# Optimization experiments

Hardware: AMD Instinct MI355X
Metric: run time of the kernel (lower is better)

The kernel has to match this reference:

```python
import jax, jax.numpy as jnp
import numpy as np

N_TOKEN = 267735
D_PROJ = 1024
CUTOFF_ENDS = [0, 20000, 40000, 200000, 267735]
D_EMBS = [1024, 256, 64, 16]  # d_embed // div_val**i, div_val=4
EMB_SCALE = float(D_PROJ) ** 0.5


def setup_inputs() -> dict:
    key = jax.random.key(0)
    ks = jax.random.split(key, 9)
    inp = jax.random.randint(ks[0], (8, 2048), 0, N_TOKEN)
    d = {"inp": inp}
    for i in range(4):
        size = CUTOFF_ENDS[i + 1] - CUTOFF_ENDS[i]
        de = D_EMBS[i]
        d[f"emb{i}"] = jax.random.normal(ks[1 + 2 * i], (size, de), jnp.float32) * 0.02
        d[f"proj{i}"] = jax.random.normal(ks[2 + 2 * i], (D_PROJ, de), jnp.float32) * 0.02
    return d


def reference(inp, emb0, emb1, emb2, emb3, proj0, proj1, proj2, proj3):
    embs = [emb0, emb1, emb2, emb3]
    projs = [proj0, proj1, proj2, proj3]
    flat = inp.reshape(-1)  # [T]
    out = jnp.zeros((flat.shape[0], D_PROJ), jnp.float32)
    for i in range(4):
        l, r = CUTOFF_ENDS[i], CUTOFF_ENDS[i + 1]
        mask = (flat >= l) & (flat < r)  # clusters are disjoint
        idx = jnp.clip(flat - l, 0, r - l - 1)  # in-range dummy where masked out
        # gather [T, d_emb_i] then project to [T, d_proj] (F.linear with weight [d_proj, d_emb_i])
        e = jnp.einsum('td,pd->tp', embs[i][idx], projs[i])
        out = jnp.where(mask[:, None], e, out)
    return (out * EMB_SCALE).reshape(*inp.shape, D_PROJ)
```

## Files before the change

### kernel.cpp

```cpp
#include <hip/hip_runtime.h>


#define CUT0 20000
#define CUT1 40000
#define CUT2 200000

#define PB1 (1024 * 1024)
#define PB2 (PB1 + 1024 * 256)
#define PB3 (PB2 + 1024 * 64)
#define PBEND (PB3 + 1024 * 32)

typedef __attribute__((ext_vector_type(8))) short bf16x8;
typedef __attribute__((ext_vector_type(8))) unsigned short u16x8;
typedef __attribute__((ext_vector_type(4))) float f32x4;

__device__ __forceinline__ unsigned short f2bf(float f) {
    unsigned u = __float_as_uint(f);
    u += 0x7FFFu + ((u >> 16) & 1u);
    return (unsigned short)(u >> 16);
}

__device__ __forceinline__ u16x8 cvt8(const float* __restrict__ s) {
    float4 a = *(const float4*)s;
    float4 b = *(const float4*)(s + 4);
    return (u16x8){f2bf(a.x), f2bf(a.y), f2bf(a.z), f2bf(a.w),
                   f2bf(b.x), f2bf(b.y), f2bf(b.z), f2bf(b.w)};
}

__device__ __forceinline__ void gl_lds16(const unsigned short* g, unsigned short* s) {
    __builtin_amdgcn_global_load_lds(
        (const __attribute__((address_space(1))) void*)g,
        (__attribute__((address_space(3))) void*)s, 16, 0, 0);
}

__global__ __launch_bounds__(256)
void classify_convert(const int* __restrict__ inp, unsigned* __restrict__ counters,
                      unsigned* __restrict__ lists, int T,
                      const float* __restrict__ proj0, const float* __restrict__ proj1,
                      const float* __restrict__ proj2, const float* __restrict__ proj3,
                      unsigned short* __restrict__ projbf) {
    int t = blockIdx.x * 256 + threadIdx.x;
    int lane = threadIdx.x & 63;
    bool valid = (t < T);
    int id = valid ? inp[t] : 0;
    int c = -1, l = 0;
    if (valid) {
        if (id < CUT0)      { c = 0; l = 0; }
        else if (id < CUT1) { c = 1; l = CUT0; }
        else if (id < CUT2) { c = 2; l = CUT1; }
        else                { c = 3; l = CUT2; }
    }
    #pragma unroll
    for (int i = 0; i < 4; ++i) {
        unsigned long long m = __ballot(c == i);
        if (c == i) {
            int leader = __ffsll(m) - 1;
            unsigned base = 0;
            if (lane == leader) base = atomicAdd(&counters[i], (unsigned)__popcll(m));
            base = __shfl(base, leader);
            unsigned rank = (unsigned)__popcll(m & ((1ull << lane) - 1ull));
            lists[(size_t)i * T + base + rank] = ((unsigned)t << 18) | (unsigned)(id - l);
        }
    }
    const int stride = gridDim.x * 256;
    for (int u = t; u < PBEND / 8; u += stride) {
        int base = u * 8;
        u16x8 o;
        if (base < PB1)       o = cvt8(proj0 + base);
        else if (base < PB2)  o = cvt8(proj1 + (base - PB1));
        else if (base < PB3)  o = cvt8(proj2 + (base - PB2));
        else {
            int rel = base - PB3;
            int row = rel >> 5, col = rel & 31;
            if (col < 16) o = cvt8(proj3 + row * 16 + col);
            else          o = (u16x8){0, 0, 0, 0, 0, 0, 0, 0};
        }
        *(u16x8*)(projbf + base) = o;
    }
}

__global__ __launch_bounds__(256)
void gather_bf16(const float* __restrict__ emb0, const float* __restrict__ emb1,
                 const float* __restrict__ emb2, const float* __restrict__ emb3,
                 const unsigned* __restrict__ lists, const unsigned* __restrict__ counters,
                 int T, unsigned short* __restrict__ ecomp) {
    const int c0 = (int)counters[0], c1 = (int)counters[1];
    const int c2 = (int)counters[2], c3 = (int)counters[3];
    const size_t off1 = (size_t)((c0 + 63) & ~63) * 1024;
    const size_t off2 = off1 + (size_t)((c1 + 63) & ~63) * 256;
    const size_t off3 = off2 + (size_t)((c2 + 63) & ~63) * 64;
    const int n0 = c0 << 7, n1 = c1 << 5, n2 = c2 << 3, n3 = c3 << 2;
    const int total = n0 + n1 + n2 + n3;
    const int stride = gridDim.x * 256;
    for (int u = blockIdx.x * 256 + threadIdx.x; u < total; u += stride) {
        int v = u;
        if (v < n0) {
            int r = v >> 7, j = v & 127;
            unsigned id = lists[r] & 0x3FFFFu;
            *(u16x8*)(ecomp + (size_t)r * 1024 + j * 8) = cvt8(emb0 + (size_t)id * 1024 + j * 8);
        } else if ((v -= n0) < n1) {
            int r = v >> 5, j = v & 31;
            unsigned id = lists[T + r] & 0x3FFFFu;
            *(u16x8*)(ecomp + off1 + (size_t)r * 256 + j * 8) = cvt8(emb1 + (size_t)id * 256 + j * 8);
        } else if ((v -= n1) < n2) {
            int r = v >> 3, j = v & 7;
            unsigned id = lists[2 * T + r] & 0x3FFFFu;
            *(u16x8*)(ecomp + off2 + (size_t)r * 64 + j * 8) = cvt8(emb2 + (size_t)id * 64 + j * 8);
        } else {
            v -= n2;
            int r = v >> 2, j = v & 3;
            unsigned id = lists[3 * T + r] & 0x3FFFFu;
            unsigned short* d = ecomp + off3 + (size_t)r * 32 + j * 8;
            if (j < 2) *(u16x8*)d = cvt8(emb3 + (size_t)id * 16 + j * 8);
            else       *(u16x8*)d = (u16x8){0, 0, 0, 0, 0, 0, 0, 0};
        }
    }
}


template<int KP>
__device__ __forceinline__
void tile_gemm_reg(const unsigned short* __restrict__ E, const unsigned short* __restrict__ P,
                   const unsigned* __restrict__ list, int count, int mtile, int ntile,
                   float* __restrict__ out) {
    constexpr int KST = KP / 32;
    const int m0 = mtile * 64;
    const int rows = min(64, count - m0);
    const int py = ntile * 128;
    const int tid = (int)threadIdx.x;
    const int lane = tid & 63;
    const int w  = tid >> 6;
    const int ln = lane & 15;
    const int qd = lane >> 4;

    const unsigned short* ea = E + (size_t)(m0 + w * 16 + ln) * KP + qd * 8;
    const unsigned short* pb = P + (size_t)(py + ln) * KP + qd * 8;

    f32x4 acc[8];
    #pragma unroll
    for (int ct = 0; ct < 8; ++ct) acc[ct] = (f32x4){0.f, 0.f, 0.f, 0.f};

    #pragma unroll
    for (int s = 0; s < KST; ++s) {
        bf16x8 a = *(const bf16x8*)(ea + s * 32);
        #pragma unroll
        for (int ct = 0; ct < 8; ++ct) {
            bf16x8 b = *(const bf16x8*)(pb + (size_t)ct * 16 * KP + s * 32);
            acc[ct] = __builtin_amdgcn_mfma_f32_16x16x32_bf16(a, b, acc[ct], 0, 0, 0);
        }
    }

    int trow[4];
    #pragma unroll
    for (int r = 0; r < 4; ++r) {
        int row = w * 16 + qd * 4 + r;
        trow[r] = (row < rows) ? (int)(list[m0 + row] >> 18) : -1;
    }
    #pragma unroll
    for (int ct = 0; ct < 8; ++ct)
        #pragma unroll
        for (int r = 0; r < 4; ++r)
            if (trow[r] >= 0)
                out[(size_t)trow[r] * 1024 + py + ct * 16 + ln] = acc[ct][r] * 32.0f;
}

template<int KP>
__device__ __forceinline__
void tile_gemm_lds(const unsigned short* __restrict__ E, const unsigned short* __restrict__ P,
                   const unsigned* __restrict__ list, int count, int mtile, int ntile,
                   float* __restrict__ out,
                   unsigned short* E_s, unsigned short* P_s, unsigned* pk_s) {
    constexpr int NCH = KP / 64;
    const int m0 = mtile * 64;
    const int rows = min(64, count - m0);
    const int py = ntile * 128;
    const int tid = (int)threadIdx.x;
    const int lane = tid & 63;
    const int w  = tid >> 6;
    const int ln = lane & 15;
    const int qd = lane >> 4;

    if (tid < 64) pk_s[tid] = (tid < rows) ? list[m0 + tid] : 0u;

    const unsigned short* eb = E + (size_t)m0 * KP;
    const unsigned short* pg = P + (size_t)py * KP;

    auto STAGE = [&](int h, int ch) {
        const int k0 = ch * 64;
        #pragma unroll
        for (int it = 0; it < 2; ++it) {
            int i16 = it * 256 + tid;
            int row = i16 >> 3, cc = (i16 & 7) ^ (row & 7);
            gl_lds16(eb + (size_t)row * KP + k0 + cc * 8, E_s + h * (64 * 64) + i16 * 8);
        }
        #pragma unroll
        for (int it = 0; it < 4; ++it) {
            int i16 = it * 256 + tid;
            int row = i16 >> 3, cc = (i16 & 7) ^ (row & 7);
            gl_lds16(pg + (size_t)row * KP + k0 + cc * 8, P_s + h * (128 * 64) + i16 * 8);
        }
    };

    f32x4 acc[8];
    #pragma unroll
    for (int ct = 0; ct < 8; ++ct) acc[ct] = (f32x4){0.f, 0.f, 0.f, 0.f};

    STAGE(0, 0);
    __syncthreads();
    int cur = 0;
    for (int ch = 0; ch < NCH; ++ch) {
        if (ch + 1 < NCH) STAGE(cur ^ 1, ch + 1);
        const unsigned short* Eb = E_s + cur * (64 * 64);
        const unsigned short* Pb = P_s + cur * (128 * 64);
        const int ar = w * 16 + ln;
        #pragma unroll
        for (int s = 0; s < 2; ++s) {
            bf16x8 a = *(const bf16x8*)(Eb + ar * 64 + (((s * 4 + qd) ^ (ar & 7)) * 8));
            #pragma unroll
            for (int ct = 0; ct < 8; ++ct) {
                const int br = ct * 16 + ln;
                bf16x8 b = *(const bf16x8*)(Pb + br * 64 + (((s * 4 + qd) ^ (br & 7)) * 8));
                acc[ct] = __builtin_amdgcn_mfma_f32_16x16x32_bf16(a, b, acc[ct], 0, 0, 0);
            }
        }
        __syncthreads();
        cur ^= 1;
    }

    #pragma unroll
    for (int ct = 0; ct < 8; ++ct) {
        #pragma unroll
        for (int r = 0; r < 4; ++r) {
            int row = w * 16 + qd * 4 + r;
            if (row < rows) {
                int t = (int)(pk_s[row] >> 18);
                out[(size_t)t * 1024 + py + ct * 16 + ln] = acc[ct][r] * 32.0f;
            }
        }
    }
    __syncthreads();
}

__global__ __launch_bounds__(256)
void gemm_fused(const unsigned short* __restrict__ ecomp, const unsigned short* __restrict__ projbf,
                const unsigned* __restrict__ lists, const unsigned* __restrict__ counters,
                int T, float* __restrict__ out) {
    __shared__ unsigned short E_s[2 * 64 * 64];
    __shared__ unsigned short P_s[2 * 128 * 64];
    __shared__ unsigned pk_s[64];

    const int c0 = (int)counters[0], c1 = (int)counters[1];
    const int c2 = (int)counters[2], c3 = (int)counters[3];
    const size_t off1 = (size_t)((c0 + 63) & ~63) * 1024;
    const size_t off2 = off1 + (size_t)((c1 + 63) & ~63) * 256;
    const size_t off3 = off2 + (size_t)((c2 + 63) & ~63) * 64;
    const int g0 = (c0 + 63) >> 6;
    const int g1 = g0 + ((c1 + 63) >> 6);
    const int g2 = g1 + ((c2 + 63) >> 6);
    const int g3 = g2 + ((c3 + 63) >> 6);

    const int xcd = blockIdx.x & 7;
    const int slot = blockIdx.x >> 3;
    const int nslots = gridDim.x >> 3;

    for (int i = slot; ; i += nslots) {
        const int g = ((i >> 3) << 3) + xcd;
        if (g >= g3) break;
        const int nt = i & 7;
        if (g < g0)      tile_gemm_lds<1024>(ecomp,        projbf,       lists,         c0, g,      nt, out, E_s, P_s, pk_s);
        else if (g < g1) tile_gemm_lds< 256>(ecomp + off1, projbf + PB1, lists + T,     c1, g - g0, nt, out, E_s, P_s, pk_s);
        else if (g < g2) tile_gemm_reg<  64>(ecomp + off2, projbf + PB2, lists + 2 * T, c2, g - g1, nt, out);
        else             tile_gemm_reg<  32>(ecomp + off3, projbf + PB3, lists + 3 * T, c3, g - g2, nt, out);
    }
}

extern "C" void kernel_launch(void* const* d_in, const int* in_sizes, int n_in,
                              void* d_out, int out_size, void* d_ws, size_t ws_size,
                              hipStream_t stream) {
    const int*   inp   = (const int*)d_in[0];
    const float* emb0  = (const float*)d_in[1];
    const float* proj0 = (const float*)d_in[2];
    const float* emb1  = (const float*)d_in[3];
    const float* proj1 = (const float*)d_in[4];
    const float* emb2  = (const float*)d_in[5];
    const float* proj2 = (const float*)d_in[6];
    const float* emb3  = (const float*)d_in[7];
    const float* proj3 = (const float*)d_in[8];
    float* out = (float*)d_out;
    const int T = in_sizes[0];

    unsigned* counters = (unsigned*)d_ws;
    unsigned* lists    = (unsigned*)((char*)d_ws + 256);
    size_t lists_b = ((size_t)4 * T * 4 + 255) & ~(size_t)255;
    unsigned short* projbf = (unsigned short*)((char*)d_ws + 256 + lists_b);
    unsigned short* ecomp  = projbf + PBEND;

    hipMemsetAsync(counters, 0, 16, stream);
    classify_convert<<<dim3(512), 256, 0, stream>>>(inp, counters, lists, T,
                                                    proj0, proj1, proj2, proj3, projbf);
    gather_bf16<<<dim3(1024), 256, 0, stream>>>(emb0, emb1, emb2, emb3,
                                                lists, counters, T, ecomp);
    gemm_fused<<<dim3(768), 256, 0, stream>>>(ecomp, projbf, lists, counters, T, out);
}
```

Baseline: 215.4 us.

## Fuse gather into GEMM for shallow clusters and split into separate kernel

```diff
diff --git a/kernel.cpp b/kernel.cpp
--- a/kernel.cpp
+++ b/kernel.cpp
@@ -81,16 +81,12 @@
 
 __global__ __launch_bounds__(256)
 void gather_bf16(const float* __restrict__ emb0, const float* __restrict__ emb1,
-                 const float* __restrict__ emb2, const float* __restrict__ emb3,
                  const unsigned* __restrict__ lists, const unsigned* __restrict__ counters,
                  int T, unsigned short* __restrict__ ecomp) {
     const int c0 = (int)counters[0], c1 = (int)counters[1];
-    const int c2 = (int)counters[2], c3 = (int)counters[3];
     const size_t off1 = (size_t)((c0 + 63) & ~63) * 1024;
-    const size_t off2 = off1 + (size_t)((c1 + 63) & ~63) * 256;
-    const size_t off3 = off2 + (size_t)((c2 + 63) & ~63) * 64;
-    const int n0 = c0 << 7, n1 = c1 << 5, n2 = c2 << 3, n3 = c3 << 2;
-    const int total = n0 + n1 + n2 + n3;
+    const int n0 = c0 << 7, n1 = c1 << 5;
+    const int total = n0 + n1;
     const int stride = gridDim.x * 256;
     for (int u = blockIdx.x * 256 + threadIdx.x; u < total; u += stride) {
         int v = u;
@@ -98,32 +94,21 @@
             int r = v >> 7, j = v & 127;
             unsigned id = lists[r] & 0x3FFFFu;
             *(u16x8*)(ecomp + (size_t)r * 1024 + j * 8) = cvt8(emb0 + (size_t)id * 1024 + j * 8);
-        } else if ((v -= n0) < n1) {
+        } else {
+            v -= n0;
             int r = v >> 5, j = v & 31;
             unsigned id = lists[T + r] & 0x3FFFFu;
             *(u16x8*)(ecomp + off1 + (size_t)r * 256 + j * 8) = cvt8(emb1 + (size_t)id * 256 + j * 8);
-        } else if ((v -= n1) < n2) {
-            int r = v >> 3, j = v & 7;
-            unsigned id = lists[2 * T + r] & 0x3FFFFu;
-            *(u16x8*)(ecomp + off2 + (size_t)r * 64 + j * 8) = cvt8(emb2 + (size_t)id * 64 + j * 8);
-        } else {
-            v -= n2;
-            int r = v >> 2, j = v & 3;
-            unsigned id = lists[3 * T + r] & 0x3FFFFu;
-            unsigned short* d = ecomp + off3 + (size_t)r * 32 + j * 8;
-            if (j < 2) *(u16x8*)d = cvt8(emb3 + (size_t)id * 16 + j * 8);
-            else       *(u16x8*)d = (u16x8){0, 0, 0, 0, 0, 0, 0, 0};
-        }
-    }
-}
-
-
-template<int KP>
+        }
+    }
+}
+
+template<int EK, int PK>
 __device__ __forceinline__
-void tile_gemm_reg(const unsigned short* __restrict__ E, const unsigned short* __restrict__ P,
-                   const unsigned* __restrict__ list, int count, int mtile, int ntile,
-                   float* __restrict__ out) {
-    constexpr int KST = KP / 32;
+void tile_shallow(const float* __restrict__ Ef, const unsigned short* __restrict__ P,
+                  const unsigned* __restrict__ list, int count, int mtile, int ntile,
+                  float* __restrict__ out) {
+    constexpr int KST = PK / 32;
     const int m0 = mtile * 64;
     const int rows = min(64, count - m0);
     const int py = ntile * 128;
@@ -133,8 +118,10 @@
     const int ln = lane & 15;
     const int qd = lane >> 4;
 
-    const unsigned short* ea = E + (size_t)(m0 + w * 16 + ln) * KP + qd * 8;
-    const unsigned short* pb = P + (size_t)(py + ln) * KP + qd * 8;
+    const int arow = w * 16 + ln;
+    const unsigned aid = (arow < rows) ? (list[m0 + arow] & 0x3FFFFu) : 0u;
+    const float* ea = Ef + (size_t)aid * EK;
+    const unsigned short* pb = P + (size_t)(py + ln) * PK + qd * 8;
 
     f32x4 acc[8];
     #pragma unroll
@@ -142,10 +129,14 @@
 
     #pragma unroll
     for (int s = 0; s < KST; ++s) {
-        bf16x8 a = *(const bf16x8*)(ea + s * 32);
+        const int k = s * 32 + qd * 8;
+        u16x8 av;
+        if (k + 8 <= EK) av = cvt8(ea + k);
+        else             av = (u16x8){0, 0, 0, 0, 0, 0, 0, 0};
+        bf16x8 a = *(const bf16x8*)&av;
         #pragma unroll
         for (int ct = 0; ct < 8; ++ct) {
-            bf16x8 b = *(const bf16x8*)(pb + (size_t)ct * 16 * KP + s * 32);
+            bf16x8 b = *(const bf16x8*)(pb + (size_t)ct * 16 * PK + s * 32);
             acc[ct] = __builtin_amdgcn_mfma_f32_16x16x32_bf16(a, b, acc[ct], 0, 0, 0);
         }
     }
@@ -162,6 +153,28 @@
         for (int r = 0; r < 4; ++r)
             if (trow[r] >= 0)
                 out[(size_t)trow[r] * 1024 + py + ct * 16 + ln] = acc[ct][r] * 32.0f;
+}
+
+__global__ __launch_bounds__(256)
+void gemm_shallow(const float* __restrict__ emb2, const float* __restrict__ emb3,
+                  const unsigned short* __restrict__ projbf,
+                  const unsigned* __restrict__ lists, const unsigned* __restrict__ counters,
+                  int T, float* __restrict__ out) {
+    const int c2 = (int)counters[2], c3 = (int)counters[3];
+    const int g2 = (c2 + 63) >> 6;
+    const int gt = g2 + ((c3 + 63) >> 6);
+
+    const int xcd = blockIdx.x & 7;
+    const int slot = blockIdx.x >> 3;
+    const int nslots = gridDim.x >> 3;
+
+    for (int i = slot; ; i += nslots) {
+        const int g = ((i >> 3) << 3) + xcd;
+        if (g >= gt) break;
+        const int nt = i & 7;
+        if (g < g2) tile_shallow<64, 64>(emb2, projbf + PB2, lists + 2 * T, c2, g,      nt, out);
+        else        tile_shallow<16, 32>(emb3, projbf + PB3, lists + 3 * T, c3, g - g2, nt, out);
+    }
 }
 
 template<int KP>
@@ -242,22 +255,17 @@
 }
 
 __global__ __launch_bounds__(256)
-void gemm_fused(const unsigned short* __restrict__ ecomp, const unsigned short* __restrict__ projbf,
-                const unsigned* __restrict__ lists, const unsigned* __restrict__ counters,
-                int T, float* __restrict__ out) {
+void gemm_deep(const unsigned short* __restrict__ ecomp, const unsigned short* __restrict__ projbf,
+               const unsigned* __restrict__ lists, const unsigned* __restrict__ counters,
+               int T, float* __restrict__ out) {
     __shared__ unsigned short E_s[2 * 64 * 64];
     __shared__ unsigned short P_s[2 * 128 * 64];
     __shared__ unsigned pk_s[64];
 
     const int c0 = (int)counters[0], c1 = (int)counters[1];
-    const int c2 = (int)counters[2], c3 = (int)counters[3];
     const size_t off1 = (size_t)((c0 + 63) & ~63) * 1024;
-    const size_t off2 = off1 + (size_t)((c1 + 63) & ~63) * 256;
-    const size_t off3 = off2 + (size_t)((c2 + 63) & ~63) * 64;
     const int g0 = (c0 + 63) >> 6;
-    const int g1 = g0 + ((c1 + 63) >> 6);
-    const int g2 = g1 + ((c2 + 63) >> 6);
-    const int g3 = g2 + ((c3 + 63) >> 6);
+    const int gt = g0 + ((c1 + 63) >> 6);
 
     const int xcd = blockIdx.x & 7;
     const int slot = blockIdx.x >> 3;
@@ -265,12 +273,10 @@
 
     for (int i = slot; ; i += nslots) {
         const int g = ((i >> 3) << 3) + xcd;
-        if (g >= g3) break;
+        if (g >= gt) break;
         const int nt = i & 7;
-        if (g < g0)      tile_gemm_lds<1024>(ecomp,        projbf,       lists,         c0, g,      nt, out, E_s, P_s, pk_s);
-        else if (g < g1) tile_gemm_lds< 256>(ecomp + off1, projbf + PB1, lists + T,     c1, g - g0, nt, out, E_s, P_s, pk_s);
-        else if (g < g2) tile_gemm_reg<  64>(ecomp + off2, projbf + PB2, lists + 2 * T, c2, g - g1, nt, out);
-        else             tile_gemm_reg<  32>(ecomp + off3, projbf + PB3, lists + 3 * T, c3, g - g2, nt, out);
+        if (g < g0) tile_gemm_lds<1024>(ecomp,        projbf,       lists,     c0, g,      nt, out, E_s, P_s, pk_s);
+        else        tile_gemm_lds< 256>(ecomp + off1, projbf + PB1, lists + T, c1, g - g0, nt, out, E_s, P_s, pk_s);
     }
 }
 
@@ -298,7 +304,7 @@
     hipMemsetAsync(counters, 0, 16, stream);
     classify_convert<<<dim3(512), 256, 0, stream>>>(inp, counters, lists, T,
                                                     proj0, proj1, proj2, proj3, projbf);
-    gather_bf16<<<dim3(1024), 256, 0, stream>>>(emb0, emb1, emb2, emb3,
-                                                lists, counters, T, ecomp);
-    gemm_fused<<<dim3(768), 256, 0, stream>>>(ecomp, projbf, lists, counters, T, out);
-}
+    gather_bf16<<<dim3(768), 256, 0, stream>>>(emb0, emb1, lists, counters, T, ecomp);
+    gemm_shallow<<<dim3(2048), 256, 0, stream>>>(emb2, emb3, projbf, lists, counters, T, out);
+    gemm_deep<<<dim3(768), 256, 0, stream>>>(ecomp, projbf, lists, counters, T, out);
+}
```

Result: slower. 226.2 us (+5.0%).
